# Kernel tuning notes

Hardware: AMD Instinct MI355X
Metric: run time of the kernel (lower is better)

## Reference

```python
import jax, jax.numpy as jnp
import numpy as np

NUM_CAPSULES = 10
NUM_ROUTES = 4096  # 64 * 8 * 8
IN_CHANNELS = 8
OUT_CHANNELS = 16
BATCH = 128
NUM_ITERATIONS = 3


def squash(s):
    # s: [B, C, O]; squash along capsule-vector dim O (torch dim=-2 of [B,1,C,O,1])
    squared_norm = jnp.sum(s * s, axis=-1, keepdims=True)
    return squared_norm * s / ((1.0 + squared_norm) * jnp.sqrt(squared_norm))


def setup_inputs() -> dict:
    key = jax.random.key(0)
    k1, k2, k3 = jax.random.split(key, 3)
    x = jax.random.normal(k1, (BATCH, NUM_ROUTES, IN_CHANNELS), dtype=jnp.float32)
    W = 0.01 * jax.random.normal(k2, (NUM_ROUTES, NUM_CAPSULES, OUT_CHANNELS, IN_CHANNELS), dtype=jnp.float32)
    bias = 0.01 * jax.random.normal(k3, (NUM_CAPSULES, OUT_CHANNELS), dtype=jnp.float32)
    return {"x": x, "W": W, "bias": bias}


def reference(x, W, bias):
    # u_hat[b,r,c,o] = sum_i W[r,c,o,i] * x[b,r,i]
    u_hat = jnp.einsum('rcoi,bri->brco', W, x)  # [B,R,C,O]
    B = x.shape[0]
    b_ij = jnp.zeros((B, NUM_ROUTES, NUM_CAPSULES), dtype=u_hat.dtype)
    v = None
    for it in range(NUM_ITERATIONS):
        c_ij = jax.nn.softmax(b_ij, axis=2)                    # softmax over capsules
        s = jnp.einsum('brc,brco->bco', c_ij, u_hat) + bias    # [B,C,O]
        v = squash(s)                                          # [B,C,O]
        if it < NUM_ITERATIONS - 1:
            a = jnp.einsum('brco,bco->brc', u_hat, v)          # agreement
            b_ij = b_ij + a
    # torch returns v_j.squeeze(1): [B, C, O, 1]
    return v[..., None]
```

## Files before the change

### kernel.cpp

```cpp
#include <hip/hip_runtime.h>
#include <math.h>

constexpr int B  = 128;
constexpr int R  = 4096;
constexpr int IC = 8;
constexpr int C  = 10;
constexpr int O  = 16;
constexpr int CO = C * O;

constexpr int RCH    = 16;
constexpr int NCHUNK = R / RCH;
constexpr int NWCONV = (R * C * O * IC) / 1024;
constexpr int NXPOSE = (R / 16) * (B / 16);

using f16x8 = __attribute__((ext_vector_type(8))) _Float16;
using f16x4 = __attribute__((ext_vector_type(4))) _Float16;
using f32x4 = __attribute__((ext_vector_type(4))) float;

template<int CTRL>
__device__ __forceinline__ float dpp_add(float v) {
    return v + __int_as_float(__builtin_amdgcn_update_dpp(
        0, __float_as_int(v), CTRL, 0xF, 0xF, true));
}
__device__ __forceinline__ float rowsum16(float v) {
    v = dpp_add<0x121>(v); v = dpp_add<0x122>(v);
    v = dpp_add<0x124>(v); v = dpp_add<0x128>(v);
    return v;
}

__device__ __forceinline__ float sum_kb(float p) {
    p += __int_as_float(__builtin_amdgcn_ds_swizzle(__float_as_int(p), 0x401F));
    p += __shfl_xor(p, 32, 64);
    return p;
}

__global__ __launch_bounds__(256)
void convert_kernel(const float* __restrict__ x, const float* __restrict__ W,
                    _Float16* __restrict__ W16, _Float16* __restrict__ xT16)
{
    const int bid = blockIdx.x;
    const int tid = threadIdx.x;
    if (bid < NWCONV) {
        const size_t i = ((size_t)bid * 256 + tid) * 4;
        float4 v = *reinterpret_cast<const float4*>(W + i);
        f16x4 h = {(_Float16)v.x, (_Float16)v.y, (_Float16)v.z, (_Float16)v.w};
        *reinterpret_cast<f16x4*>(W16 + i) = h;
    } else {
        __shared__ float tile[16][16][IC + 1];
        const int v  = bid - NWCONV;
        const int r0 = (v & 255) * 16;
        const int b0 = (v >> 8) * 16;
        {
            const int rj = tid & 15, bi = tid >> 4;
            const float* src = x + ((size_t)(b0 + bi) * R + (r0 + rj)) * IC;
            float4 a0 = *reinterpret_cast<const float4*>(src);
            float4 a1 = *reinterpret_cast<const float4*>(src + 4);
            float* t = tile[bi][rj];
            t[0]=a0.x; t[1]=a0.y; t[2]=a0.z; t[3]=a0.w;
            t[4]=a1.x; t[5]=a1.y; t[6]=a1.z; t[7]=a1.w;
        }
        __syncthreads();
        {
            const int bi = tid & 15, rj = tid >> 4;
            const float* t = tile[bi][rj];
            f16x8 h;
            #pragma unroll
            for (int i = 0; i < IC; ++i) h[i] = (_Float16)t[i];
            *reinterpret_cast<f16x8*>(xT16 + ((size_t)(r0 + rj) * B + (b0 + bi)) * IC) = h;
        }
    }
}

__global__ __launch_bounds__(256, 4)
void pass0_gemm(const _Float16* __restrict__ W16, const _Float16* __restrict__ xT16,
                float* __restrict__ s_part)
{
    const int tid = threadIdx.x;
    const int wv  = tid >> 6;
    const int l   = tid & 63;
    const int ln  = l & 15;
    const int kb  = l >> 4;

    const int g     = blockIdx.x;
    const int xcd   = g & 7;
    const int t     = g >> 3;
    const int bhalf = t & 1;
    const int cid   = t >> 1;
    const int chunk = xcd * 32 + cid;
    const int b     = bhalf * 64 + wv * 16 + ln;
    const int r0    = chunk * RCH;

    f32x4 sacc[C];
    #pragma unroll
    for (int c = 0; c < C; ++c) sacc[c] = (f32x4){0.f, 0.f, 0.f, 0.f};

    const _Float16* xptr = xT16 + ((size_t)(r0 + kb) * B + b) * IC;
    const _Float16* wptr = W16 + ((size_t)(r0 + kb) * C * O + ln) * IC;

    #pragma unroll 2
    for (int rp = 0; rp < RCH / 4; ++rp) {
        const f16x8 bf = *reinterpret_cast<const f16x8*>(xptr);
        xptr += (size_t)4 * B * IC;
        #pragma unroll
        for (int c = 0; c < C; ++c) {
            f16x8 af = *reinterpret_cast<const f16x8*>(wptr + (size_t)c * (O * IC));
            sacc[c] = __builtin_amdgcn_mfma_f32_16x16x32_f16(af, bf, sacc[c], 0, 0, 0);
        }
        wptr += (size_t)4 * C * O * IC;
    }

    float* sp = s_part + ((size_t)chunk * B + b) * CO + kb * 4;
    #pragma unroll
    for (int c = 0; c < C; ++c)
        *reinterpret_cast<float4*>(sp + c * O) =
            make_float4(sacc[c][0] * 0.1f, sacc[c][1] * 0.1f,
                        sacc[c][2] * 0.1f, sacc[c][3] * 0.1f);
}

template<int IT>
__global__ __launch_bounds__(256, 2)
void pass_mfma(const _Float16* __restrict__ W16, const _Float16* __restrict__ xT16,
               const float* __restrict__ vsum, float* __restrict__ s_part)
{
    __shared__ _Float16 wlds[RCH * C * O * IC];
    __shared__ _Float16 xlds[RCH * 64 * IC];

    const int tid = threadIdx.x;
    const int wv  = tid >> 6;
    const int l   = tid & 63;
    const int ln  = l & 15;
    const int kb  = l >> 4;

    const int g     = blockIdx.x;
    const int xcd   = g & 7;
    const int t     = g >> 3;
    const int bhalf = t & 1;
    const int cid   = t >> 1;
    const int chunk = xcd * 32 + cid;
    const int b     = bhalf * 64 + wv * 16 + ln;
    const int r0    = chunk * RCH;

    {
        const _Float16* wsrc = W16 + (size_t)r0 * (C * O * IC);
        #pragma unroll
        for (int k = 0; k < 10; ++k) {
            const int idx = (k * 256 + tid) * 8;
            *reinterpret_cast<f16x8*>(&wlds[idx]) =
                *reinterpret_cast<const f16x8*>(wsrc + idx);
        }
    }
    {
        const int rr = tid >> 6, lx = tid & 63;
        #pragma unroll
        for (int k = 0; k < 4; ++k) {
            const int r = rr + k * 4;
            *reinterpret_cast<f16x8*>(&xlds[(r * 64 + lx) * IC]) =
                *reinterpret_cast<const f16x8*>(
                    xT16 + ((size_t)(r0 + r) * B + bhalf * 64 + lx) * IC);
        }
    }

    float vreg[C][4];
    #pragma unroll
    for (int c = 0; c < C; ++c)
        *reinterpret_cast<float4*>(vreg[c]) =
            *reinterpret_cast<const float4*>(vsum + (size_t)b * CO + c * O + kb * 4);

    f32x4 sacc[C];
    #pragma unroll
    for (int c = 0; c < C; ++c) sacc[c] = (f32x4){0.f, 0.f, 0.f, 0.f};

    __syncthreads();

    const int bloc = wv * 16 + ln;

    #pragma unroll 2
    for (int rr = 0; rr < RCH; ++rr) {
        f16x8 bf;
        #pragma unroll
        for (int j = 0; j < 8; ++j) bf[j] = (_Float16)0.f;
        if (kb == 0)
            bf = *reinterpret_cast<const f16x8*>(&xlds[(rr * 64 + bloc) * IC]);

        f32x4 uh[C];
        #pragma unroll
        for (int c = 0; c < C; ++c) {
            f16x8 af = *reinterpret_cast<const f16x8*>(
                &wlds[((rr * C + c) * O + ln) * IC]);
            uh[c] = __builtin_amdgcn_mfma_f32_16x16x32_f16(
                        af, bf, (f32x4){0.f, 0.f, 0.f, 0.f}, 0, 0, 0);
        }

        float a[C];
        #pragma unroll
        for (int c = 0; c < C; ++c) {
            float p = uh[c][0] * vreg[c][0];
            p = fmaf(uh[c][1], vreg[c][1], p);
            p = fmaf(uh[c][2], vreg[c][2], p);
            p = fmaf(uh[c][3], vreg[c][3], p);
            a[c] = sum_kb(p);
        }
        float sum = 0.f;
        #pragma unroll
        for (int c = 0; c < C; ++c) { a[c] = __expf(a[c]); sum += a[c]; }
        const float inv = __builtin_amdgcn_rcpf(sum);
        #pragma unroll
        for (int c = 0; c < C; ++c) {
            const float wgt = a[c] * inv;
            #pragma unroll
            for (int j = 0; j < 4; ++j)
                sacc[c][j] = fmaf(wgt, uh[c][j], sacc[c][j]);
        }
    }

    float* sp = s_part + ((size_t)chunk * B + b) * CO + kb * 4;
    #pragma unroll
    for (int c = 0; c < C; ++c)
        *reinterpret_cast<float4*>(sp + c * O) =
            make_float4(sacc[c][0], sacc[c][1], sacc[c][2], sacc[c][3]);
}

__global__ __launch_bounds__(256)
void reduce_squash(const float* __restrict__ s_part, const float* __restrict__ bias,
                   const float* __restrict__ vin_sum,
                   float* __restrict__ v_out, float* __restrict__ vsum_out)
{
    const int b = blockIdx.x;
    const int c = blockIdx.y;
    const int t = threadIdx.x;
    const int o = t & 15;
    const int q = t >> 4;

    float acc = 0.f;
    for (int k = 0; k < NCHUNK / 16; ++k) {
        const int blk = q * (NCHUNK / 16) + k;
        acc += s_part[((size_t)blk * B + b) * CO + c * O + o];
    }
    __shared__ float red[16][O];
    red[q][o] = acc;
    __syncthreads();

    if (t < O) {
        float s = bias[c * O + o];
        #pragma unroll
        for (int k = 0; k < 16; ++k) s += red[k][o];
        float n = rowsum16(s * s);
        float v = s * sqrtf(n) / (1.f + n);
        const size_t idx = (size_t)b * CO + c * O + o;
        if (v_out)    v_out[idx] = v;
        if (vsum_out) vsum_out[idx] = (vin_sum ? vin_sum[idx] : 0.f) + v;
    }
}

extern "C" void kernel_launch(void* const* d_in, const int* in_sizes, int n_in,
                              void* d_out, int out_size, void* d_ws, size_t ws_size,
                              hipStream_t stream)
{
    const float* x    = (const float*)d_in[0];
    const float* W    = (const float*)d_in[1];
    const float* bias = (const float*)d_in[2];
    float* out = (float*)d_out;

    float* ws     = (float*)d_ws;
    float* s_part = ws;
    float* vsumA  = s_part + (size_t)NCHUNK * B * CO;
    float* vsumB  = vsumA + (size_t)B * CO;
    _Float16* W16  = (_Float16*)(vsumB + (size_t)B * CO);
    _Float16* xT16 = W16 + (size_t)R * C * O * IC;

    convert_kernel<<<NWCONV + NXPOSE, 256, 0, stream>>>(x, W, W16, xT16);

    dim3 pg(NCHUNK * 2);
    dim3 rg(B, C);

    pass0_gemm<<<pg, 256, 0, stream>>>(W16, xT16, s_part);
    reduce_squash<<<rg, 256, 0, stream>>>(s_part, bias, nullptr, nullptr, vsumA);
    pass_mfma<1><<<pg, 256, 0, stream>>>(W16, xT16, vsumA, s_part);
    reduce_squash<<<rg, 256, 0, stream>>>(s_part, bias, vsumA, nullptr, vsumB);
    pass_mfma<2><<<pg, 256, 0, stream>>>(W16, xT16, vsumB, s_part);
    reduce_squash<<<rg, 256, 0, stream>>>(s_part, bias, nullptr, out, nullptr);
}
```

Baseline: 90.68 us.

## Switch routing passes to 32x32 MFMA with fp16 partial sums

Rewrites the routing pass to use 32x32x16 MFMA tiles covering two capsules per instruction. Each block now handles a half-chunk of 8 routes across all 128 batch entries, and the pass recomputes u_hat with a second MFMA instead of keeping it in registers. Partial sums are stored as fp16 instead of fp32, halving the traffic into the reduction, and the reduction takes a runtime chunk count. The aim is to cut MFMA count, cross-lane shuffles and memory traffic, at the cost of fp16 precision in the partials and duplicated MFMA work.

```diff
diff --git a/kernel.cpp b/kernel.cpp
--- a/kernel.cpp
+++ b/kernel.cpp
@@ -10,12 +10,14 @@
 
 constexpr int RCH    = 16;
 constexpr int NCHUNK = R / RCH;
+constexpr int RH     = 8;
 constexpr int NWCONV = (R * C * O * IC) / 1024;
 constexpr int NXPOSE = (R / 16) * (B / 16);
 
-using f16x8 = __attribute__((ext_vector_type(8))) _Float16;
-using f16x4 = __attribute__((ext_vector_type(4))) _Float16;
-using f32x4 = __attribute__((ext_vector_type(4))) float;
+using f16x8  = __attribute__((ext_vector_type(8)))  _Float16;
+using f16x4  = __attribute__((ext_vector_type(4)))  _Float16;
+using f32x4  = __attribute__((ext_vector_type(4)))  float;
+using f32x16 = __attribute__((ext_vector_type(16))) float;
 
 template<int CTRL>
 __device__ __forceinline__ float dpp_add(float v) {
@@ -26,12 +28,6 @@
     v = dpp_add<0x121>(v); v = dpp_add<0x122>(v);
     v = dpp_add<0x124>(v); v = dpp_add<0x128>(v);
     return v;
-}
-
-__device__ __forceinline__ float sum_kb(float p) {
-    p += __int_as_float(__builtin_amdgcn_ds_swizzle(__float_as_int(p), 0x401F));
-    p += __shfl_xor(p, 32, 64);
-    return p;
 }
 
 __global__ __launch_bounds__(256)
@@ -73,7 +69,7 @@
 
 __global__ __launch_bounds__(256, 4)
 void pass0_gemm(const _Float16* __restrict__ W16, const _Float16* __restrict__ xT16,
-                float* __restrict__ s_part)
+                _Float16* __restrict__ s_part)
 {
     const int tid = threadIdx.x;
     const int wv  = tid >> 6;
@@ -109,132 +105,159 @@
         wptr += (size_t)4 * C * O * IC;
     }
 
-    float* sp = s_part + ((size_t)chunk * B + b) * CO + kb * 4;
-    #pragma unroll
-    for (int c = 0; c < C; ++c)
-        *reinterpret_cast<float4*>(sp + c * O) =
-            make_float4(sacc[c][0] * 0.1f, sacc[c][1] * 0.1f,
-                        sacc[c][2] * 0.1f, sacc[c][3] * 0.1f);
+    _Float16* sp = s_part + ((size_t)chunk * B + b) * CO + kb * 4;
+    #pragma unroll
+    for (int c = 0; c < C; ++c) {
+        f16x4 h = {(_Float16)(sacc[c][0] * 0.1f), (_Float16)(sacc[c][1] * 0.1f),
+                   (_Float16)(sacc[c][2] * 0.1f), (_Float16)(sacc[c][3] * 0.1f)};
+        *reinterpret_cast<f16x4*>(sp + c * O) = h;
+    }
 }
 
 template<int IT>
 __global__ __launch_bounds__(256, 2)
-void pass_mfma(const _Float16* __restrict__ W16, const _Float16* __restrict__ xT16,
-               const float* __restrict__ vsum, float* __restrict__ s_part)
-{
-    __shared__ _Float16 wlds[RCH * C * O * IC];
-    __shared__ _Float16 xlds[RCH * 64 * IC];
+void pass_mfma32(const _Float16* __restrict__ W16, const _Float16* __restrict__ xT16,
+                 const float* __restrict__ vsum, _Float16* __restrict__ s_part)
+{
+    __shared__ _Float16 wlds[RH * C * O * IC];
+    __shared__ _Float16 xlds[RH * B * IC];
 
     const int tid = threadIdx.x;
-    const int wv  = tid >> 6;
+    const int w   = tid >> 6;
     const int l   = tid & 63;
-    const int ln  = l & 15;
-    const int kb  = l >> 4;
+    const int col = l & 31;
+    const int hi  = l >> 5;
 
     const int g     = blockIdx.x;
     const int xcd   = g & 7;
     const int t     = g >> 3;
-    const int bhalf = t & 1;
+    const int rh    = t & 1;
     const int cid   = t >> 1;
     const int chunk = xcd * 32 + cid;
-    const int b     = bhalf * 64 + wv * 16 + ln;
-    const int r0    = chunk * RCH;
+    const int r0    = chunk * RCH + rh * RH;
+    const int b     = w * 32 + col;
+    const int slot  = chunk * 2 + rh;
 
     {
         const _Float16* wsrc = W16 + (size_t)r0 * (C * O * IC);
         #pragma unroll
-        for (int k = 0; k < 10; ++k) {
+        for (int k = 0; k < 5; ++k) {
             const int idx = (k * 256 + tid) * 8;
             *reinterpret_cast<f16x8*>(&wlds[idx]) =
                 *reinterpret_cast<const f16x8*>(wsrc + idx);
         }
-    }
-    {
-        const int rr = tid >> 6, lx = tid & 63;
+        const _Float16* xsrc = xT16 + (size_t)r0 * B * IC;
         #pragma unroll
         for (int k = 0; k < 4; ++k) {
-            const int r = rr + k * 4;
-            *reinterpret_cast<f16x8*>(&xlds[(r * 64 + lx) * IC]) =
-                *reinterpret_cast<const f16x8*>(
-                    xT16 + ((size_t)(r0 + r) * B + bhalf * 64 + lx) * IC);
-        }
-    }
-
-    float vreg[C][4];
-    #pragma unroll
-    for (int c = 0; c < C; ++c)
-        *reinterpret_cast<float4*>(vreg[c]) =
-            *reinterpret_cast<const float4*>(vsum + (size_t)b * CO + c * O + kb * 4);
-
-    f32x4 sacc[C];
-    #pragma unroll
-    for (int c = 0; c < C; ++c) sacc[c] = (f32x4){0.f, 0.f, 0.f, 0.f};
+            const int idx = (k * 256 + tid) * 8;
+            *reinterpret_cast<f16x8*>(&xlds[idx]) =
+                *reinterpret_cast<const f16x8*>(xsrc + idx);
+        }
+    }
+
+    float vreg[C][8];
+    #pragma unroll
+    for (int c = 0; c < C; ++c) {
+        *reinterpret_cast<float4*>(&vreg[c][0]) =
+            *reinterpret_cast<const float4*>(vsum + (size_t)b * CO + c * O + 4 * hi);
+        *reinterpret_cast<float4*>(&vreg[c][4]) =
+            *reinterpret_cast<const float4*>(vsum + (size_t)b * CO + c * O + 8 + 4 * hi);
+    }
+
+    f32x16 zero16;
+    #pragma unroll
+    for (int j = 0; j < 16; ++j) zero16[j] = 0.f;
+    f32x16 sacc[5];
+    #pragma unroll
+    for (int cp = 0; cp < 5; ++cp) sacc[cp] = zero16;
 
     __syncthreads();
 
-    const int bloc = wv * 16 + ln;
-
-    #pragma unroll 2
-    for (int rr = 0; rr < RCH; ++rr) {
+    #pragma unroll 1
+    for (int rr = 0; rr < RH; ++rr) {
         f16x8 bf;
         #pragma unroll
         for (int j = 0; j < 8; ++j) bf[j] = (_Float16)0.f;
-        if (kb == 0)
-            bf = *reinterpret_cast<const f16x8*>(&xlds[(rr * 64 + bloc) * IC]);
-
-        f32x4 uh[C];
-        #pragma unroll
-        for (int c = 0; c < C; ++c) {
-            f16x8 af = *reinterpret_cast<const f16x8*>(
-                &wlds[((rr * C + c) * O + ln) * IC]);
-            uh[c] = __builtin_amdgcn_mfma_f32_16x16x32_f16(
-                        af, bf, (f32x4){0.f, 0.f, 0.f, 0.f}, 0, 0, 0);
+        if (hi == 0)
+            bf = *reinterpret_cast<const f16x8*>(&xlds[(rr * B + b) * IC]);
+
+        f16x8 af[5];
+        #pragma unroll
+        for (int cp = 0; cp < 5; ++cp) {
+            #pragma unroll
+            for (int j = 0; j < 8; ++j) af[cp][j] = (_Float16)0.f;
+            if (hi == 0)
+                af[cp] = *reinterpret_cast<const f16x8*>(
+                    &wlds[((rr * C + cp * 2 + (col >> 4)) * O + (col & 15)) * IC]);
         }
 
         float a[C];
         #pragma unroll
-        for (int c = 0; c < C; ++c) {
-            float p = uh[c][0] * vreg[c][0];
-            p = fmaf(uh[c][1], vreg[c][1], p);
-            p = fmaf(uh[c][2], vreg[c][2], p);
-            p = fmaf(uh[c][3], vreg[c][3], p);
-            a[c] = sum_kb(p);
-        }
+        for (int cp = 0; cp < 5; ++cp) {
+            f32x16 uh = __builtin_amdgcn_mfma_f32_32x32x16_f16(af[cp], bf, zero16, 0, 0, 0);
+            float pe = 0.f, po = 0.f;
+            #pragma unroll
+            for (int j = 0; j < 8; ++j) {
+                pe = fmaf(uh[j],     vreg[cp * 2][j],     pe);
+                po = fmaf(uh[8 + j], vreg[cp * 2 + 1][j], po);
+            }
+            a[cp * 2]     = pe + __shfl_xor(pe, 32, 64);
+            a[cp * 2 + 1] = po + __shfl_xor(po, 32, 64);
+        }
+
         float sum = 0.f;
         #pragma unroll
         for (int c = 0; c < C; ++c) { a[c] = __expf(a[c]); sum += a[c]; }
         const float inv = __builtin_amdgcn_rcpf(sum);
-        #pragma unroll
-        for (int c = 0; c < C; ++c) {
-            const float wgt = a[c] * inv;
+
+        #pragma unroll
+        for (int cp = 0; cp < 5; ++cp) {
+            f32x16 uh = __builtin_amdgcn_mfma_f32_32x32x16_f16(af[cp], bf, zero16, 0, 0, 0);
+            const float we = a[cp * 2] * inv;
+            const float wo = a[cp * 2 + 1] * inv;
             #pragma unroll
-            for (int j = 0; j < 4; ++j)
-                sacc[c][j] = fmaf(wgt, uh[c][j], sacc[c][j]);
-        }
-    }
-
-    float* sp = s_part + ((size_t)chunk * B + b) * CO + kb * 4;
-    #pragma unroll
-    for (int c = 0; c < C; ++c)
-        *reinterpret_cast<float4*>(sp + c * O) =
-            make_float4(sacc[c][0], sacc[c][1], sacc[c][2], sacc[c][3]);
+            for (int j = 0; j < 8; ++j) {
+                sacc[cp][j]     = fmaf(we, uh[j],     sacc[cp][j]);
+                sacc[cp][8 + j] = fmaf(wo, uh[8 + j], sacc[cp][8 + j]);
+            }
+        }
+    }
+
+    _Float16* sp = s_part + ((size_t)slot * B + b) * CO;
+    #pragma unroll
+    for (int cp = 0; cp < 5; ++cp) {
+        const int c0 = cp * 2, c1 = cp * 2 + 1;
+        f16x4 h0 = {(_Float16)sacc[cp][0],  (_Float16)sacc[cp][1],
+                    (_Float16)sacc[cp][2],  (_Float16)sacc[cp][3]};
+        f16x4 h1 = {(_Float16)sacc[cp][4],  (_Float16)sacc[cp][5],
+                    (_Float16)sacc[cp][6],  (_Float16)sacc[cp][7]};
+        f16x4 h2 = {(_Float16)sacc[cp][8],  (_Float16)sacc[cp][9],
+                    (_Float16)sacc[cp][10], (_Float16)sacc[cp][11]};
+        f16x4 h3 = {(_Float16)sacc[cp][12], (_Float16)sacc[cp][13],
+                    (_Float16)sacc[cp][14], (_Float16)sacc[cp][15]};
+        *reinterpret_cast<f16x4*>(sp + c0 * O + 4 * hi)     = h0;
+        *reinterpret_cast<f16x4*>(sp + c0 * O + 8 + 4 * hi) = h1;
+        *reinterpret_cast<f16x4*>(sp + c1 * O + 4 * hi)     = h2;
+        *reinterpret_cast<f16x4*>(sp + c1 * O + 8 + 4 * hi) = h3;
+    }
 }
 
 __global__ __launch_bounds__(256)
-void reduce_squash(const float* __restrict__ s_part, const float* __restrict__ bias,
+void reduce_squash(const _Float16* __restrict__ s_part, const float* __restrict__ bias,
                    const float* __restrict__ vin_sum,
-                   float* __restrict__ v_out, float* __restrict__ vsum_out)
+                   float* __restrict__ v_out, float* __restrict__ vsum_out, int nch)
 {
     const int b = blockIdx.x;
     const int c = blockIdx.y;
     const int t = threadIdx.x;
     const int o = t & 15;
     const int q = t >> 4;
+    const int per = nch >> 4;
 
     float acc = 0.f;
-    for (int k = 0; k < NCHUNK / 16; ++k) {
-        const int blk = q * (NCHUNK / 16) + k;
-        acc += s_part[((size_t)blk * B + b) * CO + c * O + o];
+    for (int k = 0; k < per; ++k) {
+        const int blk = q * per + k;
+        acc += (float)s_part[((size_t)blk * B + b) * CO + c * O + o];
     }
     __shared__ float red[16][O];
     red[q][o] = acc;
@@ -261,22 +284,22 @@
     const float* bias = (const float*)d_in[2];
     float* out = (float*)d_out;
 
-    float* ws     = (float*)d_ws;
-    float* s_part = ws;
-    float* vsumA  = s_part + (size_t)NCHUNK * B * CO;
-    float* vsumB  = vsumA + (size_t)B * CO;
-    _Float16* W16  = (_Float16*)(vsumB + (size_t)B * CO);
-    _Float16* xT16 = W16 + (size_t)R * C * O * IC;
+    float* ws      = (float*)d_ws;
+    float* vsumA   = ws;
+    float* vsumB   = vsumA + (size_t)B * CO;
+    _Float16* s_part = (_Float16*)(vsumB + (size_t)B * CO);
+    _Float16* W16    = s_part + (size_t)2 * NCHUNK * B * CO;
+    _Float16* xT16   = W16 + (size_t)R * C * O * IC;
 
     convert_kernel<<<NWCONV + NXPOSE, 256, 0, stream>>>(x, W, W16, xT16);
 
-    dim3 pg(NCHUNK * 2);
+    dim3 pg(512);
     dim3 rg(B, C);
 
     pass0_gemm<<<pg, 256, 0, stream>>>(W16, xT16, s_part);
-    reduce_squash<<<rg, 256, 0, stream>>>(s_part, bias, nullptr, nullptr, vsumA);
-    pass_mfma<1><<<pg, 256, 0, stream>>>(W16, xT16, vsumA, s_part);
-    reduce_squash<<<rg, 256, 0, stream>>>(s_part, bias, vsumA, nullptr, vsumB);
-    pass_mfma<2><<<pg, 256, 0, stream>>>(W16, xT16, vsumB, s_part);
-    reduce_squash<<<rg, 256, 0, stream>>>(s_part, bias, nullptr, out, nullptr);
-}
+    reduce_squash<<<rg, 256, 0, stream>>>(s_part, bias, nullptr, nullptr, vsumA, NCHUNK);
+    pass_mfma32<1><<<pg, 256, 0, stream>>>(W16, xT16, vsumA, s_part);
+    reduce_squash<<<rg, 256, 0, stream>>>(s_part, bias, vsumA, nullptr, vsumB, 2 * NCHUNK);
+    pass_mfma32<2><<<pg, 256, 0, stream>>>(W16, xT16, vsumB, s_part);
+    reduce_squash<<<rg, 256, 0, stream>>>(s_part, bias, nullptr, out, nullptr, 2 * NCHUNK);
+}
```

Result: slower. 114.7 us (+26.5%).
